# Kernel tuning notes

Hardware: AMD Instinct MI355X
Metric: run time of the kernel (lower is better)

Reference implementation:

```python
import jax, jax.numpy as jnp
import numpy as np

N = 512        # neuron_number
F = 256        # input_size
K = 6          # unfolding_steps
B, T = 128, 256


def setup_inputs() -> dict:
    key = jax.random.key(0)
    k1, k2, k3, k4, k5, k6, k7 = jax.random.split(key, 7)
    i = jax.random.normal(k1, (B, T, F), dtype=jnp.float32)
    delta_t = jax.random.uniform(k2, (B, T), dtype=jnp.float32)  # positive dt
    # LiquidCell parameters
    W_rec = jax.random.normal(k3, (N, N), dtype=jnp.float32) / np.sqrt(N)
    W_in = jax.random.normal(k4, (N, F), dtype=jnp.float32) / np.sqrt(F)
    b = jax.random.normal(k5, (N,), dtype=jnp.float32) * 0.01
    A = jax.random.normal(k6, (N,), dtype=jnp.float32)
    tau = jax.random.uniform(k7, (N,), dtype=jnp.float32, minval=0.5, maxval=1.5)
    return {"i": i, "delta_t": delta_t, "W_rec": W_rec, "W_in": W_in,
            "b": b, "A": A, "tau": tau}


def _cell(x, i_t, dt, W_rec, W_in, b, A, tau):
    # Fused semi-implicit LTC solver, unfolded K times. x:[B,N] i_t:[B,F] dt:[B]
    dt_k = (dt / K)[:, None]                      # [B,1]
    inp_part = i_t @ W_in.T + b                   # [B,N], constant across unfolding
    for _ in range(K):
        f = jnp.tanh(x @ W_rec.T + inp_part)      # [B,N]
        x = (x + dt_k * f * A) / (1.0 + dt_k * (1.0 / tau + f))
    return x


def reference(i, delta_t, W_rec, W_in, b, A, tau):
    batch = i.shape[0]
    x0 = jnp.tanh(jnp.zeros((batch, N), dtype=i.dtype))  # _get_first_x

    def step(x, ts):
        i_t, dt = ts
        x_new = _cell(x, i_t, dt, W_rec, W_in, b, A, tau)
        return x_new, x_new

    xs = (jnp.swapaxes(i, 0, 1), delta_t.T)       # time-major: [T,B,F], [T,B]
    _, ys = jax.lax.scan(step, x0, xs)            # ys: [T,B,N]
    return jnp.swapaxes(ys, 0, 1)                 # [B,T,N] (stacked outputs)
```

## Files before the change

kernel.cpp:

```cpp
#include <hip/hip_runtime.h>
#include <math.h>

typedef unsigned long long ull;


#define NN 512
#define FF 256
#define KK 6
#define TT 256
#define BT 2
#define NTL 128

#define XROW 512
#define IPITCH 260
#define WIPITCH 260
#define PPITCH 17

#define DOT4(a, v) ((a).x * (v).x + (a).y * (v).y + (a).z * (v).z + (a).w * (v).w)

__global__ __launch_bounds__(512, 2) void liquid_kernel(
    const float* __restrict__ I,
    const float* __restrict__ DT,
    const float* __restrict__ Wrec,
    const float* __restrict__ Win,
    const float* __restrict__ bv, const float* __restrict__ Av,
    const float* __restrict__ tauv,
    ull* __restrict__ mbx,
    float* __restrict__ out)
{
  __shared__ __align__(16) float lds[39178];
  float* xsh = lds;
  float* iro = lds + BT * XROW;
  float* wi  = iro + BT * IPITCH;
  float* par = wi + NTL * WIPITCH;
  float* dts = par + 256 * PPITCH;

  const int blk = blockIdx.x;
  const int bt  = blk >> 2;
  const int nt  = blk & 3;
  const int tid = threadIdx.x;
  const int kc  = tid & 15;
  const int nq  = tid >> 4;
  const int n0g = nt * NTL;

  float4 wv[4][8];
  #pragma unroll
  for (int r = 0; r < 4; ++r) {
    const float* wr = Wrec + (size_t)(n0g + nq * 4 + r) * NN + kc * 32;
    #pragma unroll
    for (int j = 0; j < 8; ++j) wv[r][j] = *(const float4*)(wr + 4 * j);
  }
  for (int idx = tid; idx < NTL * FF; idx += 512) {
    const int n = idx >> 8, f = idx & 255;
    const int g = f >> 2, gs = g ^ ((g >> 3) & 7);
    wi[n * WIPITCH + gs * 4 + (f & 3)] = Win[(size_t)(n0g + n) * FF + f];
  }
  float rA = 0.f, rIT = 0.f, rB = 0.f;
  int swn = 0;
  if (tid < 256) {
    const int rn = tid & 127;
    const int n = n0g + rn;
    rA = Av[n]; rIT = 1.0f / tauv[n]; rB = bv[n];
    const int gg = n >> 2;
    swn = ((gg ^ ((gg >> 3) & 7)) << 2) | (n & 3);
  }
  for (int idx = tid; idx < BT * XROW; idx += 512) xsh[idx] = 0.f;

  const int sx  = kc & 7;
  const int gb  = (kc * 4) ^ ((kc >> 1) & 7);
  const float4* xq0 = (const float4*)xsh + kc * 8;
  const float4* xq1 = xq0 + 128;
  const float4* iq0 = (const float4*)iro;
  const float4* iq1 = iq0 + 65;
  const float4* wq  = (const float4*)wi + (nq * 4) * 65;
  const int stb = tid >> 8;
  const int stn = 2 * (tid & 255);
  const bool rem = (stn < n0g) || (stn >= n0g + NTL);
  const int stg = stn >> 2;
  float* stw = xsh + stb * XROW + ((stg ^ ((stg >> 3) & 7)) << 2) + (stn & 3);
  __syncthreads();

  int jj = 0;
  #pragma unroll 1
  for (int t = 0; t < TT; ++t) {
    if (tid < 2 * 64) {
      const int b = tid >> 6, f4 = tid & 63;
      const int gsi = f4 ^ ((f4 >> 3) & 7);
      ((float4*)iro)[b * 65 + gsi] =
          *(const float4*)&I[((size_t)(bt * BT + b) * TT + t) * FF + f4 * 4];
    }
    if (tid < BT) dts[tid] = DT[(size_t)(bt * BT + tid) * TT + t] * (1.0f / KK);
    __syncthreads();

    {
      float ai0[4] = {0.f, 0.f, 0.f, 0.f}, ai1[4] = {0.f, 0.f, 0.f, 0.f};
      #pragma unroll
      for (int j2 = 0; j2 < 4; ++j2) {
        const int gg = gb ^ j2;
        float4 w0 = wq[0 * 65 + gg];
        float4 w1 = wq[1 * 65 + gg];
        float4 w2 = wq[2 * 65 + gg];
        float4 w3 = wq[3 * 65 + gg];
        float4 xa = iq0[gg];
        float4 xb = iq1[gg];
        ai0[0] += DOT4(w0, xa); ai0[1] += DOT4(w1, xa);
        ai0[2] += DOT4(w2, xa); ai0[3] += DOT4(w3, xa);
        ai1[0] += DOT4(w0, xb); ai1[1] += DOT4(w1, xb);
        ai1[2] += DOT4(w2, xb); ai1[3] += DOT4(w3, xb);
      }
      #pragma unroll
      for (int r = 0; r < 4; ++r) {
        par[(0 * NTL + nq * 4 + r) * PPITCH + kc] = ai0[r];
        par[(1 * NTL + nq * 4 + r) * PPITCH + kc] = ai1[r];
      }
    }
    __syncthreads();
    float rInp = 0.f;
    if (tid < 256) {
      float s = rB;
      #pragma unroll
      for (int c = 0; c < 16; ++c) s += par[tid * PPITCH + c];
      rInp = s;
    }
    __syncthreads();

    #pragma unroll 1
    for (int kk = 0; kk < KK; ++kk) {
      ++jj;

      if (jj > 1 && rem) {
        const ull* src = mbx + (((size_t)bt * 2 + ((jj - 1) & 1)) << 10);
        const ull* p = src + 2 * tid;
        const unsigned want = (unsigned)(jj - 1);
        ull v0 = __hip_atomic_load(p,     __ATOMIC_RELAXED, __HIP_MEMORY_SCOPE_AGENT);
        ull v1 = __hip_atomic_load(p + 1, __ATOMIC_RELAXED, __HIP_MEMORY_SCOPE_AGENT);
        int guard = 1 << 16;
        while (((unsigned)(v0 >> 32) != want || (unsigned)(v1 >> 32) != want)
               && --guard) {
          __builtin_amdgcn_s_sleep(1);
          if ((unsigned)(v0 >> 32) != want)
            v0 = __hip_atomic_load(p,     __ATOMIC_RELAXED, __HIP_MEMORY_SCOPE_AGENT);
          if ((unsigned)(v1 >> 32) != want)
            v1 = __hip_atomic_load(p + 1, __ATOMIC_RELAXED, __HIP_MEMORY_SCOPE_AGENT);
        }
        stw[0] = __uint_as_float((unsigned)v0);
        stw[1] = __uint_as_float((unsigned)v1);
      }
      __syncthreads();

      {
        float acc0[4] = {0.f, 0.f, 0.f, 0.f}, acc1[4] = {0.f, 0.f, 0.f, 0.f};
        #pragma unroll
        for (int j = 0; j < 8; ++j) {
          float4 xv = xq0[j ^ sx];
          acc0[0] += DOT4(wv[0][j], xv); acc0[1] += DOT4(wv[1][j], xv);
          acc0[2] += DOT4(wv[2][j], xv); acc0[3] += DOT4(wv[3][j], xv);
        }
        #pragma unroll
        for (int j = 0; j < 8; ++j) {
          float4 xv = xq1[j ^ sx];
          acc1[0] += DOT4(wv[0][j], xv); acc1[1] += DOT4(wv[1][j], xv);
          acc1[2] += DOT4(wv[2][j], xv); acc1[3] += DOT4(wv[3][j], xv);
        }
        #pragma unroll
        for (int r = 0; r < 4; ++r) {
          par[(0 * NTL + nq * 4 + r) * PPITCH + kc] = acc0[r];
          par[(1 * NTL + nq * 4 + r) * PPITCH + kc] = acc1[r];
        }
      }
      __syncthreads();

      if (tid < 256) {
        float arg = rInp;
        #pragma unroll
        for (int c = 0; c < 16; ++c) arg += par[tid * PPITCH + c];
        const int rb = tid >> 7, rn = tid & 127;
        float f   = tanhf(arg);
        float dtk = dts[rb];
        float xo  = xsh[rb * XROW + swn];
        float xn  = fmaf(dtk * f, rA, xo) / fmaf(dtk, rIT + f, 1.0f);
        xsh[rb * XROW + swn] = xn;
        ull w = ((ull)(unsigned)jj << 32) | (ull)__float_as_uint(xn);
        __hip_atomic_store(mbx + (((size_t)bt * 2 + (jj & 1)) << 10) + rb * NN + n0g + rn,
                           w, __ATOMIC_RELAXED, __HIP_MEMORY_SCOPE_AGENT);
        if (kk == KK - 1)
          out[((size_t)(bt * BT + rb) * TT + t) * NN + n0g + rn] = xn;
      }
      __syncthreads();
    }
  }
}

extern "C" void kernel_launch(void* const* d_in, const int* in_sizes, int n_in,
                              void* d_out, int out_size, void* d_ws, size_t ws_size,
                              hipStream_t stream) {
  const float* I    = (const float*)d_in[0];
  const float* DT   = (const float*)d_in[1];
  const float* Wrec = (const float*)d_in[2];
  const float* Win  = (const float*)d_in[3];
  const float* bv   = (const float*)d_in[4];
  const float* Av   = (const float*)d_in[5];
  const float* tauv = (const float*)d_in[6];
  float* out = (float*)d_out;
  ull* mbx = (ull*)d_ws;

  liquid_kernel<<<256, 512, 0, stream>>>(I, DT, Wrec, Win, bv, Av, tauv, mbx, out);
}
```

Before: 3.634 ms.

## Overlap remote-state polling with local update using idle upper threads

Threads 0-255 compute the local state update while threads 256-511 poll the mailbox for the other blocks' 384 state values for the same step, with three values per thread. This removes one block-wide barrier and a separate polling phase at the start of each unfolding step. The cross-block wait now runs concurrently with the tanh and update work. The dt/K value is also loaded once per time step instead of once per unfolding step.

```diff
diff --git a/kernel.cpp b/kernel.cpp
--- a/kernel.cpp
+++ b/kernel.cpp
@@ -64,6 +64,21 @@
     const int gg = n >> 2;
     swn = ((gg ^ ((gg >> 3) & 7)) << 2) | (n & 3);
   }
+  int mo0 = 0, mo1 = 0, mo2 = 0;
+  int lo0 = 0, lo1 = 0, lo2 = 0;
+  if (tid >= 256) {
+    const int tp = tid - 256;
+    const int sb2 = tp >> 7;
+    const int i3 = (tp & 127) * 3;
+    const int n0 = i3 + 0 + ((i3 + 0) >= n0g ? 128 : 0);
+    const int n1 = i3 + 1 + ((i3 + 1) >= n0g ? 128 : 0);
+    const int n2 = i3 + 2 + ((i3 + 2) >= n0g ? 128 : 0);
+    mo0 = sb2 * NN + n0; mo1 = sb2 * NN + n1; mo2 = sb2 * NN + n2;
+    const int g0 = n0 >> 2, g1 = n1 >> 2, g2 = n2 >> 2;
+    lo0 = sb2 * XROW + (((g0 ^ ((g0 >> 3) & 7)) << 2) | (n0 & 3));
+    lo1 = sb2 * XROW + (((g1 ^ ((g1 >> 3) & 7)) << 2) | (n1 & 3));
+    lo2 = sb2 * XROW + (((g2 ^ ((g2 >> 3) & 7)) << 2) | (n2 & 3));
+  }
   for (int idx = tid; idx < BT * XROW; idx += 512) xsh[idx] = 0.f;
 
   const int sx  = kc & 7;
@@ -73,11 +88,6 @@
   const float4* iq0 = (const float4*)iro;
   const float4* iq1 = iq0 + 65;
   const float4* wq  = (const float4*)wi + (nq * 4) * 65;
-  const int stb = tid >> 8;
-  const int stn = 2 * (tid & 255);
-  const bool rem = (stn < n0g) || (stn >= n0g + NTL);
-  const int stg = stn >> 2;
-  float* stw = xsh + stb * XROW + ((stg ^ ((stg >> 3) & 7)) << 2) + (stn & 3);
   __syncthreads();
 
   int jj = 0;
@@ -115,38 +125,19 @@
       }
     }
     __syncthreads();
-    float rInp = 0.f;
+    float rInp = 0.f, dtk = 0.f;
     if (tid < 256) {
       float s = rB;
       #pragma unroll
       for (int c = 0; c < 16; ++c) s += par[tid * PPITCH + c];
       rInp = s;
+      dtk = dts[tid >> 7];
     }
     __syncthreads();
 
     #pragma unroll 1
     for (int kk = 0; kk < KK; ++kk) {
       ++jj;
-
-      if (jj > 1 && rem) {
-        const ull* src = mbx + (((size_t)bt * 2 + ((jj - 1) & 1)) << 10);
-        const ull* p = src + 2 * tid;
-        const unsigned want = (unsigned)(jj - 1);
-        ull v0 = __hip_atomic_load(p,     __ATOMIC_RELAXED, __HIP_MEMORY_SCOPE_AGENT);
-        ull v1 = __hip_atomic_load(p + 1, __ATOMIC_RELAXED, __HIP_MEMORY_SCOPE_AGENT);
-        int guard = 1 << 16;
-        while (((unsigned)(v0 >> 32) != want || (unsigned)(v1 >> 32) != want)
-               && --guard) {
-          __builtin_amdgcn_s_sleep(1);
-          if ((unsigned)(v0 >> 32) != want)
-            v0 = __hip_atomic_load(p,     __ATOMIC_RELAXED, __HIP_MEMORY_SCOPE_AGENT);
-          if ((unsigned)(v1 >> 32) != want)
-            v1 = __hip_atomic_load(p + 1, __ATOMIC_RELAXED, __HIP_MEMORY_SCOPE_AGENT);
-        }
-        stw[0] = __uint_as_float((unsigned)v0);
-        stw[1] = __uint_as_float((unsigned)v1);
-      }
-      __syncthreads();
 
       {
         float acc0[4] = {0.f, 0.f, 0.f, 0.f}, acc1[4] = {0.f, 0.f, 0.f, 0.f};
@@ -176,7 +167,6 @@
         for (int c = 0; c < 16; ++c) arg += par[tid * PPITCH + c];
         const int rb = tid >> 7, rn = tid & 127;
         float f   = tanhf(arg);
-        float dtk = dts[rb];
         float xo  = xsh[rb * XROW + swn];
         float xn  = fmaf(dtk * f, rA, xo) / fmaf(dtk, rIT + f, 1.0f);
         xsh[rb * XROW + swn] = xn;
@@ -185,6 +175,29 @@
                            w, __ATOMIC_RELAXED, __HIP_MEMORY_SCOPE_AGENT);
         if (kk == KK - 1)
           out[((size_t)(bt * BT + rb) * TT + t) * NN + n0g + rn] = xn;
+      } else if (jj < KK * TT) {
+        const ull* base = mbx + (((size_t)bt * 2 + (jj & 1)) << 10);
+        const unsigned want = (unsigned)jj;
+        ull v0 = __hip_atomic_load(base + mo0, __ATOMIC_RELAXED, __HIP_MEMORY_SCOPE_AGENT);
+        ull v1 = __hip_atomic_load(base + mo1, __ATOMIC_RELAXED, __HIP_MEMORY_SCOPE_AGENT);
+        ull v2 = __hip_atomic_load(base + mo2, __ATOMIC_RELAXED, __HIP_MEMORY_SCOPE_AGENT);
+        unsigned pend = ((unsigned)(v0 >> 32) != want ? 1u : 0u)
+                      | ((unsigned)(v1 >> 32) != want ? 2u : 0u)
+                      | ((unsigned)(v2 >> 32) != want ? 4u : 0u);
+        int guard = 1 << 16;
+        while (pend && --guard) {
+          __builtin_amdgcn_s_sleep(1);
+          ull w0, w1, w2;
+          if (pend & 1u) w0 = __hip_atomic_load(base + mo0, __ATOMIC_RELAXED, __HIP_MEMORY_SCOPE_AGENT);
+          if (pend & 2u) w1 = __hip_atomic_load(base + mo1, __ATOMIC_RELAXED, __HIP_MEMORY_SCOPE_AGENT);
+          if (pend & 4u) w2 = __hip_atomic_load(base + mo2, __ATOMIC_RELAXED, __HIP_MEMORY_SCOPE_AGENT);
+          if ((pend & 1u) && (unsigned)(w0 >> 32) == want) { v0 = w0; pend &= ~1u; }
+          if ((pend & 2u) && (unsigned)(w1 >> 32) == want) { v1 = w1; pend &= ~2u; }
+          if ((pend & 4u) && (unsigned)(w2 >> 32) == want) { v2 = w2; pend &= ~4u; }
+        }
+        xsh[lo0] = __uint_as_float((unsigned)v0);
+        xsh[lo1] = __uint_as_float((unsigned)v1);
+        xsh[lo2] = __uint_as_float((unsigned)v2);
       }
       __syncthreads();
     }
```

Result: slower. 4.041 ms (+11.2%).
